# Optimization experiments

Measured on AMD Instinct MI355X. Metric: run time of the kernel, lower is better.

Reference implementation:

```python
import jax, jax.numpy as jnp
import numpy as np

N_NODES = 50000
N_EDGES = 600000
D = 128
R = 8
EPS = 1e-5


def layer_norm(x, g, b):
    mu = jnp.mean(x, axis=-1, keepdims=True)
    var = jnp.mean(jnp.square(x - mu), axis=-1, keepdims=True)
    return (x - mu) * jax.lax.rsqrt(var + EPS) * g + b


def rgcn(x, src, dst, edge_attr, W, root, bias, num_nodes):
    # x: [N, d], W: [R, d, f], edge_attr: [E, R] soft relation weights
    E = src.shape[0]
    f = W.shape[-1]
    msg = jnp.zeros((E, f), dtype=x.dtype)
    for r in range(W.shape[0]):  # small fixed relation count
        hr = x @ W[r]                       # [N, f]
        msg = msg + hr[src] * edge_attr[:, r][:, None]  # gather + weight
    agg = jax.ops.segment_sum(msg, dst, num_segments=num_nodes)  # scatter-add
    return agg + x @ root + bias


def setup_inputs() -> dict:
    key = jax.random.key(0)
    ks = jax.random.split(key, 12)
    s = 1.0 / np.sqrt(D)
    return {
        "x": jax.random.normal(ks[0], (N_NODES, D), dtype=jnp.float32),
        "edge_index": jax.random.randint(ks[1], (2, N_EDGES), 0, N_NODES, dtype=jnp.int64),
        "edge_attr": jax.random.uniform(ks[2], (N_EDGES, R), dtype=jnp.float32),
        "ln1_g": jnp.ones((D,), jnp.float32),
        "ln1_b": jnp.zeros((D,), jnp.float32),
        "W1": jax.random.normal(ks[3], (R, D, D), jnp.float32) * s,
        "root1": jax.random.normal(ks[4], (D, D), jnp.float32) * s,
        "b1": jnp.zeros((D,), jnp.float32),
        "ln2_g": jnp.ones((D,), jnp.float32),
        "ln2_b": jnp.zeros((D,), jnp.float32),
        "W2": jax.random.normal(ks[5], (R, D, D), jnp.float32) * s,
        "root2": jax.random.normal(ks[6], (D, D), jnp.float32) * s,
        "b2": jnp.zeros((D,), jnp.float32),
    }


def reference(x, edge_index, edge_attr, ln1_g, ln1_b, W1, root1, b1,
              ln2_g, ln2_b, W2, root2, b2):
    src, dst = edge_index[0], edge_index[1]
    identity = x
    out = jax.nn.gelu(layer_norm(x, ln1_g, ln1_b), approximate=False)
    out = rgcn(out, src, dst, edge_attr, W1, root1, b1, x.shape[0])
    out = jax.nn.gelu(layer_norm(out, ln2_g, ln2_b), approximate=False)
    out = rgcn(out, src, dst, edge_attr, W2, root2, b2, x.shape[0])
    return out + identity
```

## Files before the change

kernel.cpp:

```cpp
#include <hip/hip_runtime.h>
#include <hip/hip_bf16.h>

typedef __attribute__((ext_vector_type(8))) short short8;
typedef __attribute__((ext_vector_type(4))) float f32x4;

#define LDA 1152

__device__ __forceinline__ float bf2f(unsigned short u) {
    union { unsigned int i; float f; } v; v.i = ((unsigned int)u) << 16; return v.f;
}
__device__ __forceinline__ unsigned short f2bf(float f) {
    __hip_bfloat16 h = __float2bfloat16(f);
    union { __hip_bfloat16 h; unsigned short u; } v; v.h = h; return v.u;
}
__device__ __forceinline__ float gelu_exact(float t) {
    return 0.5f * t * (1.0f + erff(t * 0.70710678118654752f));
}

__global__ void prep_w(const float* __restrict__ W1, const float* __restrict__ root1,
                       unsigned short* __restrict__ Bf1,
                       const float* __restrict__ W2, const float* __restrict__ root2,
                       unsigned short* __restrict__ Bf2,
                       int* __restrict__ cnt, int cntN) {
    int i = blockIdx.x * 256 + threadIdx.x;
    const float* W = W1; const float* root = root1; unsigned short* Bfrag = Bf1;
    if (i >= 2 * 1152 * 128) {
        int zi = i - 2 * 1152 * 128;
        if (zi < cntN) cnt[zi] = 0;
        return;
    }
    if (i >= 1152 * 128) { i -= 1152 * 128; W = W2; root = root2; Bfrag = Bf2; }
    int kp = i >> 7, n = i & 127;
    float v;
    if (kp < 1024) {
        int d = kp >> 3, r = kp & 7;
        v = W[((size_t)r * 128 + d) * 128 + n];
    } else {
        v = root[(size_t)(kp - 1024) * 128 + n];
    }
    int kb = kp >> 5;
    int lane = (((kp >> 3) & 3) << 4) | (n & 15);
    int j = kp & 7;
    int t = n >> 4;
    Bfrag[(((size_t)(kb * 8 + t) * 64 + lane) << 3) + j] = f2bf(v);
}

__global__ void hist_dst(const int* __restrict__ ei, int* __restrict__ cnt, int E) {
    int e = blockIdx.x * 256 + threadIdx.x;
    if (e >= E) return;
    atomicAdd(&cnt[ei[E + e]], 1);
}

__global__ void scan1(const int* __restrict__ cnt, int* __restrict__ part,
                      int* __restrict__ bsum, int N) {
    int i = blockIdx.x * 256 + threadIdx.x;
    int v = (i < N) ? cnt[i] : 0;
    int lane = threadIdx.x & 63, wid = threadIdx.x >> 6;
    int s = v;
    #pragma unroll
    for (int off = 1; off < 64; off <<= 1) {
        int t = __shfl_up(s, off);
        if (lane >= off) s += t;
    }
    __shared__ int wsum[4];
    if (lane == 63) wsum[wid] = s;
    __syncthreads();
    int add = 0;
    for (int w = 0; w < wid; ++w) add += wsum[w];
    s += add;
    part[i] = s - v;
    if (threadIdx.x == 255) bsum[blockIdx.x] = s;
}

__global__ void scan3(const int* __restrict__ part, const int* __restrict__ bsum,
                      int* __restrict__ rowptr, int* __restrict__ woff, int N) {
    __shared__ int base_sh;
    int b = blockIdx.x;
    if (threadIdx.x < 64) {
        int acc = 0;
        for (int j = threadIdx.x; j < b; j += 64) acc += bsum[j];
        #pragma unroll
        for (int o = 32; o; o >>= 1) acc += __shfl_xor(acc, o);
        if (threadIdx.x == 0) base_sh = acc;
    }
    __syncthreads();
    int i = b * 256 + threadIdx.x;
    if (i >= N) return;
    int v = part[i] + base_sh;
    rowptr[i] = v;
    woff[i] = v;
}

__global__ void scatter_edges(const int* __restrict__ ei, const float4* __restrict__ attr,
                              int* __restrict__ woff, int* __restrict__ esrc,
                              short8* __restrict__ eattr, int E) {
    int e = blockIdx.x * 256 + threadIdx.x;
    if (e >= E) return;
    int src = ei[e], dst = ei[E + e];
    float4 a0 = attr[2 * e], a1 = attr[2 * e + 1];
    short8 pk;
    pk[0] = (short)f2bf(a0.x); pk[1] = (short)f2bf(a0.y);
    pk[2] = (short)f2bf(a0.z); pk[3] = (short)f2bf(a0.w);
    pk[4] = (short)f2bf(a1.x); pk[5] = (short)f2bf(a1.y);
    pk[6] = (short)f2bf(a1.z); pk[7] = (short)f2bf(a1.w);
    int p = atomicAdd(&woff[dst], 1);
    esrc[p] = src;
    eattr[p] = pk;
}

__global__ void ln_gelu(const float* __restrict__ x, const float* __restrict__ g,
                        const float* __restrict__ b, unsigned short* __restrict__ A, int N) {
    int row = (blockIdx.x * blockDim.x + threadIdx.x) >> 6;
    if (row >= N) return;
    int lane = threadIdx.x & 63;
    float2 v = *(const float2*)(x + (size_t)row * 128 + lane * 2);
    float s = v.x + v.y;
    #pragma unroll
    for (int o = 32; o; o >>= 1) s += __shfl_xor(s, o);
    float mu = s * (1.0f / 128.0f);
    float d0 = v.x - mu, d1 = v.y - mu;
    float q = d0 * d0 + d1 * d1;
    #pragma unroll
    for (int o = 32; o; o >>= 1) q += __shfl_xor(q, o);
    float rs = rsqrtf(q * (1.0f / 128.0f) + 1e-5f);
    float2 gg = *(const float2*)(g + lane * 2);
    float2 bb = *(const float2*)(b + lane * 2);
    ushort2 o2;
    o2.x = f2bf(gelu_exact(d0 * rs * gg.x + bb.x));
    o2.y = f2bf(gelu_exact(d1 * rs * gg.y + bb.y));
    *(ushort2*)(A + (size_t)row * LDA + 1024 + lane * 2) = o2;
}

__global__ __launch_bounds__(256) void edge_z(const int* __restrict__ rowptr,
                                              const int* __restrict__ esrc,
                                              const short8* __restrict__ eattr,
                                              unsigned short* __restrict__ A, int N, int E) {
    int row = (blockIdx.x << 2) + (threadIdx.x >> 6);
    if (row >= N) return;
    int lane = threadIdx.x & 63;
    int e0 = rowptr[row];
    int e1 = (row + 1 < N) ? rowptr[row + 1] : E;
    float a0[8] = {0,0,0,0,0,0,0,0};
    float a1[8] = {0,0,0,0,0,0,0,0};
    const unsigned short* yl = A + 1024 + lane * 2;

    #define EDGE_FMA(hv, ea) do {                                      \
        float y0 = bf2f((unsigned short)((hv) & 0xffffu));             \
        float y1 = bf2f((unsigned short)((hv) >> 16));                 \
        _Pragma("unroll")                                              \
        for (int r = 0; r < 8; ++r) {                                  \
            float wv = bf2f((unsigned short)(ea)[r]);                  \
            a0[r] += wv * y0; a1[r] += wv * y1;                        \
        }                                                              \
    } while (0)

    int e = e0;
    for (; e + 4 <= e1; e += 4) {
        unsigned int h[4];
        short8 ea[4];
        #pragma unroll
        for (int u = 0; u < 4; ++u) {
            h[u] = *(const unsigned int*)(yl + (size_t)esrc[e + u] * LDA);
            ea[u] = eattr[e + u];
        }
        #pragma unroll
        for (int u = 0; u < 4; ++u) EDGE_FMA(h[u], ea[u]);
    }
    for (; e < e1; ++e) {
        unsigned int h = *(const unsigned int*)(yl + (size_t)esrc[e] * LDA);
        short8 ea = eattr[e];
        EDGE_FMA(h, ea);
    }
    #undef EDGE_FMA

    short8 p0, p1;
    #pragma unroll
    for (int r = 0; r < 8; ++r) { p0[r] = (short)f2bf(a0[r]); p1[r] = (short)f2bf(a1[r]); }
    unsigned short* zr = A + (size_t)row * LDA + lane * 16;
    *(short8*)zr = p0;
    *(short8*)(zr + 8) = p1;
}

template <int MODE>
__global__ __launch_bounds__(256) void gemm_fused(
        unsigned short* __restrict__ A, const unsigned short* __restrict__ Bfrag,
        const float* __restrict__ bias, const float* __restrict__ lng,
        const float* __restrict__ lnb, const float* __restrict__ xres,
        float* __restrict__ outp, int N) {
    __shared__ short8 Bs[2][1024];

    int w = threadIdx.x >> 6;
    int lane = threadIdx.x & 63;
    int l15 = lane & 15, lhi = lane >> 4;
    int m0 = blockIdx.x * 64 + w * 16;

    const unsigned short* ap = A + (size_t)(m0 + l15) * LDA + lhi * 8;
    const short8* bfb = (const short8*)Bfrag;

    #define STAGE(buf, c)                                                          \
        do {                                                                       \
            const short8* gsrc = bfb + (size_t)(c) * 1024 + w * 64;                \
            _Pragma("unroll")                                                      \
            for (int i = 0; i < 4; ++i)                                            \
                __builtin_amdgcn_global_load_lds(&gsrc[i * 256 + lane],            \
                                                 &Bs[buf][w * 64 + i * 256], 16, 0, 0); \
        } while (0)

    #define BARRIER_CNT2()                                                          \
        do {                                                                        \
            asm volatile("s_waitcnt vmcnt(2)" ::: "memory");                        \
            __builtin_amdgcn_sched_barrier(0);                                      \
            __builtin_amdgcn_s_barrier();                                           \
            __builtin_amdgcn_sched_barrier(0);                                      \
        } while (0)

    short8 af[2], afn[2];
    STAGE(0, 0);
    __builtin_amdgcn_sched_barrier(0);
    #pragma unroll
    for (int k = 0; k < 2; ++k) af[k] = *(const short8*)(ap + k * 32);
    __builtin_amdgcn_sched_barrier(0);
    BARRIER_CNT2();

    f32x4 acc[8] = {};
    for (int c = 0; c < 18; ++c) {
        int cur = c & 1;
        if (c < 17) {
            STAGE(cur ^ 1, c + 1);
            __builtin_amdgcn_sched_barrier(0);
            #pragma unroll
            for (int k = 0; k < 2; ++k)
                afn[k] = *(const short8*)(ap + ((c + 1) * 2 + k) * 32);
            __builtin_amdgcn_sched_barrier(0);
        }
        #pragma unroll
        for (int k = 0; k < 2; ++k) {
            #pragma unroll
            for (int t = 0; t < 8; ++t) {
                short8 b = Bs[cur][k * 512 + t * 64 + lane];
                acc[t] = __builtin_amdgcn_mfma_f32_16x16x32_bf16(af[k], b, acc[t], 0, 0, 0);
            }
        }
        if (c < 17) {
            BARRIER_CNT2();
            af[0] = afn[0]; af[1] = afn[1];
        }
    }
    #undef STAGE
    #undef BARRIER_CNT2

    float bcol[8];
    #pragma unroll
    for (int t = 0; t < 8; ++t) bcol[t] = bias[t * 16 + l15];

    if (MODE == 0) {
        float gcol[8], lbcol[8];
        #pragma unroll
        for (int t = 0; t < 8; ++t) { gcol[t] = lng[t * 16 + l15]; lbcol[t] = lnb[t * 16 + l15]; }
        #pragma unroll
        for (int reg = 0; reg < 4; ++reg) {
            int row = m0 + lhi * 4 + reg;
            float tv[8];
            float s = 0.f;
            #pragma unroll
            for (int t = 0; t < 8; ++t) { tv[t] = acc[t][reg] + bcol[t]; s += tv[t]; }
            #pragma unroll
            for (int msk = 1; msk < 16; msk <<= 1) s += __shfl_xor(s, msk);
            float mu = s * (1.0f / 128.0f);
            float q = 0.f;
            #pragma unroll
            for (int t = 0; t < 8; ++t) { float d = tv[t] - mu; q += d * d; }
            #pragma unroll
            for (int msk = 1; msk < 16; msk <<= 1) q += __shfl_xor(q, msk);
            float rs = rsqrtf(q * (1.0f / 128.0f) + 1e-5f);
            if (row < N) {
                #pragma unroll
                for (int t = 0; t < 8; ++t) {
                    float u = gelu_exact((tv[t] - mu) * rs * gcol[t] + lbcol[t]);
                    A[(size_t)row * LDA + 1024 + t * 16 + l15] = f2bf(u);
                }
            }
        }
    } else {
        #pragma unroll
        for (int reg = 0; reg < 4; ++reg) {
            int row = m0 + lhi * 4 + reg;
            if (row < N) {
                #pragma unroll
                for (int t = 0; t < 8; ++t) {
                    size_t idx = (size_t)row * 128 + t * 16 + l15;
                    outp[idx] = acc[t][reg] + bcol[t] + xres[idx];
                }
            }
        }
    }
}

extern "C" void kernel_launch(void* const* d_in, const int* in_sizes, int n_in,
                              void* d_out, int out_size, void* d_ws, size_t ws_size,
                              hipStream_t stream) {
    const float* x     = (const float*)d_in[0];
    const int*   ei    = (const int*)d_in[1];
    const float* attr  = (const float*)d_in[2];
    const float* ln1g  = (const float*)d_in[3];
    const float* ln1b  = (const float*)d_in[4];
    const float* W1    = (const float*)d_in[5];
    const float* root1 = (const float*)d_in[6];
    const float* b1    = (const float*)d_in[7];
    const float* ln2g  = (const float*)d_in[8];
    const float* ln2b  = (const float*)d_in[9];
    const float* W2    = (const float*)d_in[10];
    const float* root2 = (const float*)d_in[11];
    const float* b2    = (const float*)d_in[12];

    const int N = in_sizes[0] / 128;
    const int E = in_sizes[1] / 2;

    char* ws = (char*)d_ws;
    unsigned short* A     = (unsigned short*)(ws);
    unsigned short* Bf1   = (unsigned short*)(ws + 115400000);
    unsigned short* Bf2   = (unsigned short*)(ws + 115700000);
    int*            cnt   = (int*)(ws + 116000000);
    int*            part  = (int*)(ws + 116210000);
    int*            bsum  = (int*)(ws + 116420000);
    int*            rowptr= (int*)(ws + 116430000);
    int*            woff  = (int*)(ws + 116640000);
    int*            esrc  = (int*)(ws + 116850000);
    short8*         eattr = (short8*)(ws + 119250000);

    const int scanBlocks  = (N + 255) / 256;
    const int edgeBlocksE = (E + 255) / 256;
    const int rowsBlocks  = (N * 64 + 255) / 256;
    const int nodeBlocks  = (N + 3) / 4;
    const int gemmBlocks  = (N + 63) / 64;
    const int prepBlocks  = 1152 + scanBlocks;

    prep_w<<<prepBlocks, 256, 0, stream>>>(W1, root1, Bf1, W2, root2, Bf2,
                                           cnt, scanBlocks * 256);

    hist_dst<<<edgeBlocksE, 256, 0, stream>>>(ei, cnt, E);
    scan1<<<scanBlocks, 256, 0, stream>>>(cnt, part, bsum, N);
    scan3<<<scanBlocks, 256, 0, stream>>>(part, bsum, rowptr, woff, N);
    scatter_edges<<<edgeBlocksE, 256, 0, stream>>>(ei, (const float4*)attr, woff, esrc, eattr, E);

    ln_gelu<<<rowsBlocks, 256, 0, stream>>>(x, ln1g, ln1b, A, N);
    edge_z<<<nodeBlocks, 256, 0, stream>>>(rowptr, esrc, eattr, A, N, E);
    gemm_fused<0><<<gemmBlocks, 256, 0, stream>>>(A, Bf1, b1, ln2g, ln2b, nullptr, nullptr, N);

    edge_z<<<nodeBlocks, 256, 0, stream>>>(rowptr, esrc, eattr, A, N, E);
    gemm_fused<1><<<gemmBlocks, 256, 0, stream>>>(A, Bf2, b2, nullptr, nullptr, x, (float*)d_out, N);
}
```

Measured before the change: 247.1 us.

## Prefetch next edge gather batch in edge_z; shrink GEMM blocks to 32 rows

In the edge aggregation kernel, the next group of four gathered source-node values is loaded while the current group's FMAs run, a software-pipelining step meant to hide gather latency. The fused GEMM is also restructured to use 128-thread blocks covering 32 rows each, with smaller K chunks (36 stages of 32 instead of 18 of 64) and half-size shared memory staging. Smaller blocks give more blocks and better occupancy and tail balance, but double the number of barriers and the total B-fragment staging traffic per row, and the prefetch needs extra registers.

```diff
diff --git a/kernel.cpp b/kernel.cpp
--- a/kernel.cpp
+++ b/kernel.cpp
@@ -155,21 +155,35 @@
     } while (0)
 
     int e = e0;
-    for (; e + 4 <= e1; e += 4) {
-        unsigned int h[4];
-        short8 ea[4];
+    unsigned int h[4];
+    bool have = (e + 4 <= e1);
+    if (have) {
+        #pragma unroll
+        for (int u = 0; u < 4; ++u)
+            h[u] = *(const unsigned int*)(yl + (size_t)esrc[e + u] * LDA);
+    }
+    while (have) {
+        int en = e + 4;
+        bool haveN = (en + 4 <= e1);
+        unsigned int hn[4] = {0, 0, 0, 0};
+        if (haveN) {
+            #pragma unroll
+            for (int u = 0; u < 4; ++u)
+                hn[u] = *(const unsigned int*)(yl + (size_t)esrc[en + u] * LDA);
+        }
         #pragma unroll
         for (int u = 0; u < 4; ++u) {
-            h[u] = *(const unsigned int*)(yl + (size_t)esrc[e + u] * LDA);
-            ea[u] = eattr[e + u];
-        }
-        #pragma unroll
-        for (int u = 0; u < 4; ++u) EDGE_FMA(h[u], ea[u]);
+            short8 ea = eattr[e + u];
+            EDGE_FMA(h[u], ea);
+        }
+        #pragma unroll
+        for (int u = 0; u < 4; ++u) h[u] = hn[u];
+        e = en; have = haveN;
     }
     for (; e < e1; ++e) {
-        unsigned int h = *(const unsigned int*)(yl + (size_t)esrc[e] * LDA);
+        unsigned int hv = *(const unsigned int*)(yl + (size_t)esrc[e] * LDA);
         short8 ea = eattr[e];
-        EDGE_FMA(h, ea);
+        EDGE_FMA(hv, ea);
     }
     #undef EDGE_FMA
 
@@ -182,72 +196,67 @@
 }
 
 template <int MODE>
-__global__ __launch_bounds__(256) void gemm_fused(
+__global__ __launch_bounds__(128) void gemm_fused(
         unsigned short* __restrict__ A, const unsigned short* __restrict__ Bfrag,
         const float* __restrict__ bias, const float* __restrict__ lng,
         const float* __restrict__ lnb, const float* __restrict__ xres,
         float* __restrict__ outp, int N) {
-    __shared__ short8 Bs[2][1024];
+    __shared__ short8 Bs[2][512];
 
     int w = threadIdx.x >> 6;
     int lane = threadIdx.x & 63;
+    int ti = w * 64 + lane;
     int l15 = lane & 15, lhi = lane >> 4;
-    int m0 = blockIdx.x * 64 + w * 16;
+    int m0 = blockIdx.x * 32 + w * 16;
 
     const unsigned short* ap = A + (size_t)(m0 + l15) * LDA + lhi * 8;
     const short8* bfb = (const short8*)Bfrag;
 
     #define STAGE(buf, c)                                                          \
         do {                                                                       \
-            const short8* gsrc = bfb + (size_t)(c) * 1024 + w * 64;                \
+            const short8* gsrc = bfb + (size_t)(c) * 512;                          \
             _Pragma("unroll")                                                      \
             for (int i = 0; i < 4; ++i)                                            \
-                __builtin_amdgcn_global_load_lds(&gsrc[i * 256 + lane],            \
-                                                 &Bs[buf][w * 64 + i * 256], 16, 0, 0); \
+                __builtin_amdgcn_global_load_lds(&gsrc[i * 128 + ti],              \
+                                                 &Bs[buf][i * 128 + ti], 16, 0, 0); \
         } while (0)
 
-    #define BARRIER_CNT2()                                                          \
+    #define BARRIER_CNT1()                                                          \
         do {                                                                        \
-            asm volatile("s_waitcnt vmcnt(2)" ::: "memory");                        \
+            asm volatile("s_waitcnt vmcnt(1)" ::: "memory");                        \
             __builtin_amdgcn_sched_barrier(0);                                      \
             __builtin_amdgcn_s_barrier();                                           \
             __builtin_amdgcn_sched_barrier(0);                                      \
         } while (0)
 
-    short8 af[2], afn[2];
+    short8 af, afn;
     STAGE(0, 0);
     __builtin_amdgcn_sched_barrier(0);
-    #pragma unroll
-    for (int k = 0; k < 2; ++k) af[k] = *(const short8*)(ap + k * 32);
+    af = *(const short8*)ap;
     __builtin_amdgcn_sched_barrier(0);
-    BARRIER_CNT2();
+    BARRIER_CNT1();
 
     f32x4 acc[8] = {};
-    for (int c = 0; c < 18; ++c) {
+    for (int c = 0; c < 36; ++c) {
         int cur = c & 1;
-        if (c < 17) {
+        if (c < 35) {
             STAGE(cur ^ 1, c + 1);
             __builtin_amdgcn_sched_barrier(0);
-            #pragma unroll
-            for (int k = 0; k < 2; ++k)
-                afn[k] = *(const short8*)(ap + ((c + 1) * 2 + k) * 32);
+            afn = *(const short8*)(ap + (c + 1) * 32);
             __builtin_amdgcn_sched_barrier(0);
         }
         #pragma unroll
-        for (int k = 0; k < 2; ++k) {
-            #pragma unroll
-            for (int t = 0; t < 8; ++t) {
-                short8 b = Bs[cur][k * 512 + t * 64 + lane];
-                acc[t] = __builtin_amdgcn_mfma_f32_16x16x32_bf16(af[k], b, acc[t], 0, 0, 0);
-            }
-        }
-        if (c < 17) {
-            BARRIER_CNT2();
-            af[0] = afn[0]; af[1] = afn[1];
+        for (int t = 0; t < 8; ++t) {
+            short8 b = Bs[cur][t * 64 + lane];
+            acc[t] = __builtin_amdgcn_mfma_f32_16x16x32_bf16(af, b, acc[t], 0, 0, 0);
+        }
+        if (c < 35) {
+            BARRIER_CNT1();
+            af = afn;
         }
     }
     #undef STAGE
-    #undef BARRIER_CNT2
+    #undef BARRIER_CNT1
 
     float bcol[8];
     #pragma unroll
@@ -332,7 +341,7 @@
     const int edgeBlocksE = (E + 255) / 256;
     const int rowsBlocks  = (N * 64 + 255) / 256;
     const int nodeBlocks  = (N + 3) / 4;
-    const int gemmBlocks  = (N + 63) / 64;
+    const int gemmBlocks  = (N + 31) / 32;
     const int prepBlocks  = 1152 + scanBlocks;
 
     prep_w<<<prepBlocks, 256, 0, stream>>>(W1, root1, Bf1, W2, root2, Bf2,
@@ -345,8 +354,8 @@
 
     ln_gelu<<<rowsBlocks, 256, 0, stream>>>(x, ln1g, ln1b, A, N);
     edge_z<<<nodeBlocks, 256, 0, stream>>>(rowptr, esrc, eattr, A, N, E);
-    gemm_fused<0><<<gemmBlocks, 256, 0, stream>>>(A, Bf1, b1, ln2g, ln2b, nullptr, nullptr, N);
+    gemm_fused<0><<<gemmBlocks, 128, 0, stream>>>(A, Bf1, b1, ln2g, ln2b, nullptr, nullptr, N);
 
     edge_z<<<nodeBlocks, 256, 0, stream>>>(rowptr, esrc, eattr, A, N, E);
-    gemm_fused<1><<<gemmBlocks, 256, 0, stream>>>(A, Bf2, b2, nullptr, nullptr, x, (float*)d_out, N);
-}
+    gemm_fused<1><<<gemmBlocks, 128, 0, stream>>>(A, Bf2, b2, nullptr, nullptr, x, (float*)d_out, N);
+}
```

After: 274.2 us. +10.9%, slower.
